# Optimization experiments

Hardware: AMD Instinct MI355X
Metric: run time of the kernel (lower is better)

## Reference

```python
import jax, jax.numpy as jnp
import numpy as np
import math

D_MODEL = 1024
N_HEADS = 16
HEAD_DIM = D_MODEL // N_HEADS


def rotate_half(x):
    x1, x2 = x[..., : x.shape[-1] // 2], x[..., x.shape[-1] // 2 :]
    return jnp.concatenate([-x2, x1], axis=-1)


def rope_cos_sin(T, dim, dtype):
    inv_freq = 1.0 / (10000.0 ** (jnp.arange(0, dim, 2, dtype=jnp.float32) / dim))
    t = jnp.arange(T, dtype=jnp.float32)
    freqs = jnp.einsum('i,j->ij', t, inv_freq)          # [T, dim/2]
    emb = jnp.concatenate([freqs, freqs], axis=-1)      # [T, dim]
    # broadcast shape [1, T, 1, dim] to match q/k of shape [B, T, H, dim]
    return emb.astype(dtype)[None, :, None, :]


def setup_inputs() -> dict:
    key = jax.random.key(0)
    k_x, k_qkv_w, k_qkv_b, k_p_w, k_p_b = jax.random.split(key, 5)
    B, T = 2, 2048
    s = 1.0 / math.sqrt(D_MODEL)
    return {
        'x': jax.random.normal(k_x, (B, T, D_MODEL), dtype=jnp.float32),
        'qkv_w': jax.random.uniform(k_qkv_w, (3 * D_MODEL, D_MODEL), minval=-s, maxval=s, dtype=jnp.float32),
        'qkv_b': jax.random.uniform(k_qkv_b, (3 * D_MODEL,), minval=-s, maxval=s, dtype=jnp.float32),
        'proj_w': jax.random.uniform(k_p_w, (D_MODEL, D_MODEL), minval=-s, maxval=s, dtype=jnp.float32),
        'proj_b': jax.random.uniform(k_p_b, (D_MODEL,), minval=-s, maxval=s, dtype=jnp.float32),
    }


def reference(x, qkv_w, qkv_b, proj_w, proj_b):
    B, T, C = x.shape
    H, Dh = N_HEADS, HEAD_DIM
    qkv = x @ qkv_w.T + qkv_b                           # [B, T, 3C]
    qkv = qkv.reshape(B, T, 3, H, Dh)
    q, k, v = qkv[:, :, 0], qkv[:, :, 1], qkv[:, :, 2]  # [B, T, H, Dh]
    emb = rope_cos_sin(T, Dh, x.dtype)
    cos, sin = jnp.cos(emb), jnp.sin(emb)
    q = q * cos + rotate_half(q) * sin
    k = k * cos + rotate_half(k) * sin
    # attention with causal mask (dropout in eval mode = identity)
    scale = 1.0 / math.sqrt(Dh)
    attn = jnp.einsum('bqhd,bkhd->bhqk', q, k) * scale  # [B, H, T, T]
    causal = jnp.tril(jnp.ones((T, T), dtype=bool))
    attn = jnp.where(causal, attn, -jnp.inf)
    attn = jax.nn.softmax(attn, axis=-1)
    out = jnp.einsum('bhqk,bkhd->bqhd', attn, v).reshape(B, T, C)
    return out @ proj_w.T + proj_b
```

## Files before the change

### kernel.cpp

```cpp
#include <hip/hip_runtime.h>
#include <math.h>

#define T_SEQ 2048
#define NB 2
#define NH 16
#define DH 64
#define DM 1024

typedef unsigned short u16;
typedef __attribute__((ext_vector_type(8))) __bf16 bf16x8;
typedef __attribute__((ext_vector_type(4))) float f32x4;
typedef __attribute__((ext_vector_type(4))) int i32x4;

__device__ __forceinline__ u16 f2bf(float f) {
  unsigned u = __builtin_bit_cast(unsigned, f);
  u += 0x7FFFu + ((u >> 16) & 1u);
  return (u16)(u >> 16);
}
__device__ __forceinline__ float bf2f(u16 v) {
  unsigned u = ((unsigned)v) << 16;
  return __builtin_bit_cast(float, u);
}
__device__ __forceinline__ bf16x8 ld_frag(const u16* p) {
  bf16x8 r; __builtin_memcpy(&r, p, 16); return r;
}
__device__ __forceinline__ i32x4 ld16(const u16* p) {
  i32x4 r; __builtin_memcpy(&r, p, 16); return r;
}
__device__ __forceinline__ void st16(u16* p, i32x4 v) {
  __builtin_memcpy(p, &v, 16);
}
__device__ __forceinline__ void cvt_store8(u16* dst, const float* src) {
  f32x4 a, b;
  __builtin_memcpy(&a, src, 16);
  __builtin_memcpy(&b, src + 4, 16);
  u16 t[8];
  t[0] = f2bf(a[0]); t[1] = f2bf(a[1]); t[2] = f2bf(a[2]); t[3] = f2bf(a[3]);
  t[4] = f2bf(b[0]); t[5] = f2bf(b[1]); t[6] = f2bf(b[2]); t[7] = f2bf(b[3]);
  __builtin_memcpy(dst, t, 16);
}
__device__ __forceinline__ void gld_lds16(const u16* g, u16* l) {
  __builtin_amdgcn_global_load_lds(
      (const __attribute__((address_space(1))) void*)g,
      (__attribute__((address_space(3))) void*)l, 16, 0, 0);
}

__global__ __launch_bounds__(256) void cvt_f32_bf16(const float* __restrict__ in,
                                                    u16* __restrict__ out, int n8) {
  const int i = blockIdx.x * 256 + threadIdx.x;
  if (i < n8) cvt_store8(out + (long)i * 8, in + (long)i * 8);
}

template <int MODE>
__global__ __launch_bounds__(256) void gemm_nt(
    const u16* __restrict__ A, const u16* __restrict__ Bw,
    const float* __restrict__ bias, float* __restrict__ out,
    u16* __restrict__ q_ws, u16* __restrict__ k_ws, u16* __restrict__ v_ws,
    int M, int N, int K) {
  __shared__ __align__(16) u16 As[128 * 32];
  __shared__ __align__(16) u16 Bs[128 * 32];
  const int tid = threadIdx.x;
  const int wave = tid >> 6, lane = tid & 63;
  const int quad = lane >> 4, l16 = lane & 15;
  const int wm = wave & 1, wn = wave >> 1;
  const int m0 = blockIdx.y * 128, n0 = blockIdx.x * 128;
  const int lrow = lane >> 2;
  const int lcol = (lane & 3) * 8;

  f32x4 acc[4][4] = {};

  const u16* Ag = A + (long)(m0 + wave * 16 + lrow) * K + lcol;
  const u16* Bg = Bw + (long)(n0 + wave * 16 + lrow) * K + lcol;
  u16* Al = &As[(wave * 16 + lrow) * 32 + lcol];
  u16* Bl = &Bs[(wave * 16 + lrow) * 32 + lcol];

  for (int k0 = 0; k0 < K; k0 += 32) {
    __syncthreads();
    gld_lds16(Ag + k0, Al);
    gld_lds16(Ag + (long)64 * K + k0, Al + 64 * 32);
    gld_lds16(Bg + k0, Bl);
    gld_lds16(Bg + (long)64 * K + k0, Bl + 64 * 32);
    __syncthreads();
    bf16x8 af[4], bfr[4];
#pragma unroll
    for (int mt = 0; mt < 4; mt++)
      af[mt] = ld_frag(&As[(wm * 64 + mt * 16 + l16) * 32 + quad * 8]);
#pragma unroll
    for (int nt = 0; nt < 4; nt++)
      bfr[nt] = ld_frag(&Bs[(wn * 64 + nt * 16 + l16) * 32 + quad * 8]);
#pragma unroll
    for (int mt = 0; mt < 4; mt++)
#pragma unroll
      for (int nt = 0; nt < 4; nt++)
        acc[mt][nt] = __builtin_amdgcn_mfma_f32_16x16x32_bf16(af[mt], bfr[nt],
                                                              acc[mt][nt], 0, 0, 0);
  }

#pragma unroll
  for (int nt = 0; nt < 4; nt++) {
    const int col = n0 + wn * 64 + nt * 16 + l16;
    const float bv = bias[col];
    if constexpr (MODE == 1) {
#pragma unroll
      for (int mt = 0; mt < 4; mt++) {
        const int rbase = m0 + wm * 64 + mt * 16 + quad * 4;
#pragma unroll
        for (int r = 0; r < 4; r++)
          out[(long)(rbase + r) * N + col] = acc[mt][nt][r] + bv;
      }
    } else {
      const int which = col >> 10;
      const int rem = col & 1023;
      const int h = rem >> 6, dh = rem & 63;
#pragma unroll
      for (int mt = 0; mt < 4; mt++) {
        const int rbase = m0 + wm * 64 + mt * 16 + quad * 4;
#pragma unroll
        for (int r = 0; r < 4; r++) {
          const int m = rbase + r;
          const int b = m >> 11, t = m & (T_SEQ - 1);
          const u16 val = f2bf(acc[mt][nt][r] + bv);
          if (which == 0)
            q_ws[(((long)(b * NH + h)) * T_SEQ + t) * DH + dh] = val;
          else if (which == 1)
            k_ws[(((long)(b * NH + h)) * T_SEQ + t) * DH + dh] = val;
          else
            v_ws[(((long)(b * NH + h)) * DH + dh) * T_SEQ + t] = val;
        }
      }
    }
  }
}

__global__ __launch_bounds__(256) void rope_kernel(u16* __restrict__ q,
                                                   u16* __restrict__ k) {
  const int idx = blockIdx.x * 256 + threadIdx.x;
  const int i = idx & 31;
  const int t = (idx >> 5) & (T_SEQ - 1);
  const int bh = idx >> 16;
  const long base = ((long)bh * T_SEQ + t) * DH;
  const float invf = exp2f(-(float)i * 0.41524101186092045f);
  const float ang = (float)t * invf;
  const float c = cosf(ang), s = sinf(ang);
  const float q1 = bf2f(q[base + i]), q2 = bf2f(q[base + i + 32]);
  const float k1 = bf2f(k[base + i]), k2 = bf2f(k[base + i + 32]);
  q[base + i]      = f2bf((q1 * c - q2 * s) * 0.125f);
  q[base + i + 32] = f2bf((q2 * c + q1 * s) * 0.125f);
  k[base + i]      = f2bf(k1 * c - k2 * s);
  k[base + i + 32] = f2bf(k2 * c + k1 * s);
}

__global__ __launch_bounds__(256) void attn_kernel(const u16* __restrict__ q,
                                                   const u16* __restrict__ k,
                                                   const u16* __restrict__ v,
                                                   u16* __restrict__ o) {
  __shared__ __align__(16) u16 Ks[128 * 72];
  __shared__ __align__(16) u16 Vt[64 * 136];
  __shared__ __align__(16) u16 Pbuf[4][16 * 136];
  const int tid = threadIdx.x;
  const int wave = tid >> 6, lane = tid & 63;
  const int quad = lane >> 4, l16 = lane & 15;
  const int bh = blockIdx.x;
  const int y = blockIdx.y;
  const int qt = (y & 1) ? (31 - (y >> 1)) : (y >> 1);
  const long base = (long)bh * T_SEQ * DH;
  const int b = bh >> 4, h = bh & 15;

  const int q0 = qt * 64;
  bf16x8 aq0, aq1;
  {
    const u16* qr = q + base + (long)(q0 + wave * 16 + l16) * DH + quad * 8;
    aq0 = ld_frag(qr);
    aq1 = ld_frag(qr + 32);
  }
  float mst[4], lst[4];
  f32x4 oacc[4] = {};
#pragma unroll
  for (int r = 0; r < 4; r++) { mst[r] = -1e30f; lst[r] = 0.f; }
  const int row_g = q0 + wave * 16 + quad * 4;
  const int nkt = (q0 + 64 + 127) >> 7;

  for (int kt = 0; kt < nkt; kt++) {
    const int key0 = kt * 128;
    __syncthreads();
    {
      const u16* kp = k + base + (long)key0 * DH;
#pragma unroll
      for (int p = 0; p < 4; p++) {
        const int rr = (tid >> 3) + p * 32;
        const int cc = (tid & 7) * 8;
        st16(&Ks[rr * 72 + cc], ld16(kp + rr * 64 + cc));
      }
      const u16* vp = v + base + key0;
#pragma unroll
      for (int p = 0; p < 4; p++) {
        const int d = (tid >> 4) + p * 16;
        const int cc = (tid & 15) * 8;
        st16(&Vt[d * 136 + cc], ld16(vp + (long)d * T_SEQ + cc));
      }
    }
    __syncthreads();

    f32x4 sfr[8];
#pragma unroll
    for (int nt = 0; nt < 8; nt++) {
      bf16x8 b0 = ld_frag(&Ks[(nt * 16 + l16) * 72 + quad * 8]);
      bf16x8 b1 = ld_frag(&Ks[(nt * 16 + l16) * 72 + 32 + quad * 8]);
      f32x4 z = {0.f, 0.f, 0.f, 0.f};
      z = __builtin_amdgcn_mfma_f32_16x16x32_bf16(aq0, b0, z, 0, 0, 0);
      z = __builtin_amdgcn_mfma_f32_16x16x32_bf16(aq1, b1, z, 0, 0, 0);
      sfr[nt] = z;
    }

    if (kt == nkt - 1) {
#pragma unroll
      for (int nt = 0; nt < 8; nt++) {
        const int colg = key0 + nt * 16 + l16;
#pragma unroll
        for (int r = 0; r < 4; r++)
          sfr[nt][r] = (colg <= row_g + r) ? sfr[nt][r] : -1e30f;
      }
    }

    float rmax[4];
#pragma unroll
    for (int r = 0; r < 4; r++) {
      float m = sfr[0][r];
#pragma unroll
      for (int nt = 1; nt < 8; nt++) m = fmaxf(m, sfr[nt][r]);
      rmax[r] = m;
    }
#pragma unroll
    for (int off = 1; off < 16; off <<= 1)
#pragma unroll
      for (int r = 0; r < 4; r++)
        rmax[r] = fmaxf(rmax[r], __shfl_xor(rmax[r], off, 64));

    float alpha[4], rsum[4];
#pragma unroll
    for (int r = 0; r < 4; r++) {
      const float mnew = fmaxf(mst[r], rmax[r]);
      alpha[r] = exp2f((mst[r] - mnew) * 1.44269504f);
      mst[r] = mnew;
      rsum[r] = 0.f;
    }
#pragma unroll
    for (int nt = 0; nt < 8; nt++) {
#pragma unroll
      for (int r = 0; r < 4; r++) {
        const float p = exp2f((sfr[nt][r] - mst[r]) * 1.44269504f);
        rsum[r] += p;
        Pbuf[wave][(quad * 4 + r) * 136 + nt * 16 + l16] = f2bf(p);
      }
    }
#pragma unroll
    for (int off = 1; off < 16; off <<= 1)
#pragma unroll
      for (int r = 0; r < 4; r++) rsum[r] += __shfl_xor(rsum[r], off, 64);
#pragma unroll
    for (int r = 0; r < 4; r++) lst[r] = lst[r] * alpha[r] + rsum[r];
#pragma unroll
    for (int ont = 0; ont < 4; ont++)
#pragma unroll
      for (int r = 0; r < 4; r++) oacc[ont][r] *= alpha[r];

    asm volatile("s_waitcnt lgkmcnt(0)" ::: "memory");

    bf16x8 ap[4];
#pragma unroll
    for (int c = 0; c < 4; c++)
      ap[c] = ld_frag(&Pbuf[wave][l16 * 136 + c * 32 + quad * 8]);
#pragma unroll
    for (int ont = 0; ont < 4; ont++) {
#pragma unroll
      for (int c = 0; c < 4; c++) {
        bf16x8 bv = ld_frag(&Vt[(ont * 16 + l16) * 136 + c * 32 + quad * 8]);
        oacc[ont] = __builtin_amdgcn_mfma_f32_16x16x32_bf16(ap[c], bv, oacc[ont], 0, 0, 0);
      }
    }
  }

#pragma unroll
  for (int ont = 0; ont < 4; ont++) {
#pragma unroll
    for (int r = 0; r < 4; r++) {
      const float val = oacc[ont][r] / lst[r];
      const int row = row_g + r;
      o[((long)(b * T_SEQ + row)) * DM + h * DH + ont * 16 + l16] = f2bf(val);
    }
  }
}

extern "C" void kernel_launch(void* const* d_in, const int* in_sizes, int n_in,
                              void* d_out, int out_size, void* d_ws, size_t ws_size,
                              hipStream_t stream) {
  const float* x      = (const float*)d_in[0];
  const float* qkv_w  = (const float*)d_in[1];
  const float* qkv_b  = (const float*)d_in[2];
  const float* proj_w = (const float*)d_in[3];
  const float* proj_b = (const float*)d_in[4];
  float* out = (float*)d_out;

  u16* ws = (u16*)d_ws;
  const long per = (long)NB * NH * T_SEQ * DH;
  u16* q_ws = ws;
  u16* k_ws = ws + per;
  u16* v_ws = ws + 2 * per;
  u16* ao_ws = ws + 3 * per;
  u16* x_bf  = ws + 3 * per;
  u16* w_bf  = ws + 4 * per;

  dim3 blk(256);
  cvt_f32_bf16<<<2048, blk, 0, stream>>>(x, x_bf, (int)(per / 8));
  cvt_f32_bf16<<<1536, blk, 0, stream>>>(qkv_w, w_bf, 3 * DM * DM / 8);
  gemm_nt<0><<<dim3(24, 32), blk, 0, stream>>>(x_bf, w_bf, qkv_b, nullptr,
                                               q_ws, k_ws, v_ws, 4096, 3072, 1024);
  rope_kernel<<<8192, blk, 0, stream>>>(q_ws, k_ws);
  attn_kernel<<<dim3(32, 32), blk, 0, stream>>>(q_ws, k_ws, v_ws, ao_ws);
  cvt_f32_bf16<<<512, blk, 0, stream>>>(proj_w, w_bf, DM * DM / 8);
  gemm_nt<1><<<dim3(8, 32), blk, 0, stream>>>(ao_ws, w_bf, proj_b, out,
                                              nullptr, nullptr, nullptr, 4096, 1024, 1024);
}
```

Before: 230.7 us.

## Compute transposed S tile so P stays in registers, dropping LDS round-trip

The attention kernel now computes S^T (keys as MFMA rows, queries as columns), so each lane owns one query row. The softmax row max and sum then need only two cross-lane shuffles instead of four per row. The P fragments are fed straight from registers into 16x16x16 bf16 MFMAs against V^T, removing the per-wave Pbuf LDS write, wait and reload. This trades the 16x16x32 MFMA for twice as many smaller MFMAs in the PV product, and output stores become 8-byte writes per lane.

New measurement: 245.5 us. +6.4%, slower.

```diff
diff --git a/kernel.cpp b/kernel.cpp
--- a/kernel.cpp
+++ b/kernel.cpp
@@ -9,6 +9,7 @@
 
 typedef unsigned short u16;
 typedef __attribute__((ext_vector_type(8))) __bf16 bf16x8;
+typedef __attribute__((ext_vector_type(4))) short s16x4;
 typedef __attribute__((ext_vector_type(4))) float f32x4;
 typedef __attribute__((ext_vector_type(4))) int i32x4;
 
@@ -23,6 +24,9 @@
 }
 __device__ __forceinline__ bf16x8 ld_frag(const u16* p) {
   bf16x8 r; __builtin_memcpy(&r, p, 16); return r;
+}
+__device__ __forceinline__ s16x4 ld8(const u16* p) {
+  s16x4 r; __builtin_memcpy(&r, p, 8); return r;
 }
 __device__ __forceinline__ i32x4 ld16(const u16* p) {
   i32x4 r; __builtin_memcpy(&r, p, 16); return r;
@@ -156,7 +160,6 @@
                                                    u16* __restrict__ o) {
   __shared__ __align__(16) u16 Ks[128 * 72];
   __shared__ __align__(16) u16 Vt[64 * 136];
-  __shared__ __align__(16) u16 Pbuf[4][16 * 136];
   const int tid = threadIdx.x;
   const int wave = tid >> 6, lane = tid & 63;
   const int quad = lane >> 4, l16 = lane & 15;
@@ -167,17 +170,15 @@
   const int b = bh >> 4, h = bh & 15;
 
   const int q0 = qt * 64;
-  bf16x8 aq0, aq1;
+  const int qrow = q0 + wave * 16 + l16;
+  bf16x8 bq0, bq1;
   {
-    const u16* qr = q + base + (long)(q0 + wave * 16 + l16) * DH + quad * 8;
-    aq0 = ld_frag(qr);
-    aq1 = ld_frag(qr + 32);
-  }
-  float mst[4], lst[4];
+    const u16* qr = q + base + (long)qrow * DH + quad * 8;
+    bq0 = ld_frag(qr);
+    bq1 = ld_frag(qr + 32);
+  }
+  float mst = -1e30f, lst = 0.f;
   f32x4 oacc[4] = {};
-#pragma unroll
-  for (int r = 0; r < 4; r++) { mst[r] = -1e30f; lst[r] = 0.f; }
-  const int row_g = q0 + wave * 16 + quad * 4;
   const int nkt = (q0 + 64 + 127) >> 7;
 
   for (int kt = 0; kt < nkt; kt++) {
@@ -204,90 +205,75 @@
     f32x4 sfr[8];
 #pragma unroll
     for (int nt = 0; nt < 8; nt++) {
-      bf16x8 b0 = ld_frag(&Ks[(nt * 16 + l16) * 72 + quad * 8]);
-      bf16x8 b1 = ld_frag(&Ks[(nt * 16 + l16) * 72 + 32 + quad * 8]);
+      bf16x8 k0f = ld_frag(&Ks[(nt * 16 + l16) * 72 + quad * 8]);
+      bf16x8 k1f = ld_frag(&Ks[(nt * 16 + l16) * 72 + 32 + quad * 8]);
       f32x4 z = {0.f, 0.f, 0.f, 0.f};
-      z = __builtin_amdgcn_mfma_f32_16x16x32_bf16(aq0, b0, z, 0, 0, 0);
-      z = __builtin_amdgcn_mfma_f32_16x16x32_bf16(aq1, b1, z, 0, 0, 0);
+      z = __builtin_amdgcn_mfma_f32_16x16x32_bf16(k0f, bq0, z, 0, 0, 0);
+      z = __builtin_amdgcn_mfma_f32_16x16x32_bf16(k1f, bq1, z, 0, 0, 0);
       sfr[nt] = z;
     }
 
     if (kt == nkt - 1) {
 #pragma unroll
       for (int nt = 0; nt < 8; nt++) {
-        const int colg = key0 + nt * 16 + l16;
+        const int keyb = key0 + nt * 16 + quad * 4;
 #pragma unroll
         for (int r = 0; r < 4; r++)
-          sfr[nt][r] = (colg <= row_g + r) ? sfr[nt][r] : -1e30f;
-      }
-    }
-
-    float rmax[4];
-#pragma unroll
-    for (int r = 0; r < 4; r++) {
-      float m = sfr[0][r];
-#pragma unroll
-      for (int nt = 1; nt < 8; nt++) m = fmaxf(m, sfr[nt][r]);
-      rmax[r] = m;
-    }
-#pragma unroll
-    for (int off = 1; off < 16; off <<= 1)
-#pragma unroll
-      for (int r = 0; r < 4; r++)
-        rmax[r] = fmaxf(rmax[r], __shfl_xor(rmax[r], off, 64));
-
-    float alpha[4], rsum[4];
-#pragma unroll
-    for (int r = 0; r < 4; r++) {
-      const float mnew = fmaxf(mst[r], rmax[r]);
-      alpha[r] = exp2f((mst[r] - mnew) * 1.44269504f);
-      mst[r] = mnew;
-      rsum[r] = 0.f;
-    }
+          sfr[nt][r] = (keyb + r <= qrow) ? sfr[nt][r] : -1e30f;
+      }
+    }
+
+    float rmax = sfr[0][0];
+#pragma unroll
+    for (int nt = 0; nt < 8; nt++)
+#pragma unroll
+      for (int r = 0; r < 4; r++) rmax = fmaxf(rmax, sfr[nt][r]);
+    rmax = fmaxf(rmax, __shfl_xor(rmax, 16, 64));
+    rmax = fmaxf(rmax, __shfl_xor(rmax, 32, 64));
+
+    const float mnew = fmaxf(mst, rmax);
+    const float alpha = exp2f((mst - mnew) * 1.44269504f);
+    mst = mnew;
+
+    float rsum = 0.f;
+    s16x4 pf[8];
 #pragma unroll
     for (int nt = 0; nt < 8; nt++) {
 #pragma unroll
       for (int r = 0; r < 4; r++) {
-        const float p = exp2f((sfr[nt][r] - mst[r]) * 1.44269504f);
-        rsum[r] += p;
-        Pbuf[wave][(quad * 4 + r) * 136 + nt * 16 + l16] = f2bf(p);
-      }
-    }
-#pragma unroll
-    for (int off = 1; off < 16; off <<= 1)
-#pragma unroll
-      for (int r = 0; r < 4; r++) rsum[r] += __shfl_xor(rsum[r], off, 64);
-#pragma unroll
-    for (int r = 0; r < 4; r++) lst[r] = lst[r] * alpha[r] + rsum[r];
+        const float p = exp2f((sfr[nt][r] - mnew) * 1.44269504f);
+        rsum += p;
+        pf[nt][r] = (short)f2bf(p);
+      }
+    }
+    rsum += __shfl_xor(rsum, 16, 64);
+    rsum += __shfl_xor(rsum, 32, 64);
+    lst = lst * alpha + rsum;
 #pragma unroll
     for (int ont = 0; ont < 4; ont++)
 #pragma unroll
-      for (int r = 0; r < 4; r++) oacc[ont][r] *= alpha[r];
-
-    asm volatile("s_waitcnt lgkmcnt(0)" ::: "memory");
-
-    bf16x8 ap[4];
-#pragma unroll
-    for (int c = 0; c < 4; c++)
-      ap[c] = ld_frag(&Pbuf[wave][l16 * 136 + c * 32 + quad * 8]);
+      for (int r = 0; r < 4; r++) oacc[ont][r] *= alpha;
+
 #pragma unroll
     for (int ont = 0; ont < 4; ont++) {
-#pragma unroll
-      for (int c = 0; c < 4; c++) {
-        bf16x8 bv = ld_frag(&Vt[(ont * 16 + l16) * 136 + c * 32 + quad * 8]);
-        oacc[ont] = __builtin_amdgcn_mfma_f32_16x16x32_bf16(ap[c], bv, oacc[ont], 0, 0, 0);
-      }
-    }
-  }
-
+      const u16* vrow = &Vt[(ont * 16 + l16) * 136 + quad * 4];
+#pragma unroll
+      for (int nt = 0; nt < 8; nt++) {
+        s16x4 vf = ld8(vrow + nt * 16);
+        oacc[ont] = __builtin_amdgcn_mfma_f32_16x16x16bf16_1k(vf, pf[nt],
+                                                              oacc[ont], 0, 0, 0);
+      }
+    }
+  }
+
+  const float inv_l = 1.f / lst;
+  u16* orow = o + ((long)(b * T_SEQ + qrow)) * DM + h * DH + quad * 4;
 #pragma unroll
   for (int ont = 0; ont < 4; ont++) {
-#pragma unroll
-    for (int r = 0; r < 4; r++) {
-      const float val = oacc[ont][r] / lst[r];
-      const int row = row_g + r;
-      o[((long)(b * T_SEQ + row)) * DM + h * DH + ont * 16 + l16] = f2bf(val);
-    }
+    u16 t4[4];
+#pragma unroll
+    for (int r = 0; r < 4; r++) t4[r] = f2bf(oacc[ont][r] * inv_l);
+    __builtin_memcpy(orow + ont * 16, t4, 8);
   }
 }
 
```
